# Kernel tuning notes

Measured on AMD Instinct MI355X. Metric: run time of the kernel, lower is better.

The kernel has to match this reference:

```python
import jax, jax.numpy as jnp
import numpy as np

DIM = 512
HEADS = 4
MARGIN = 1.0


def _attn_pool(x, Wq, bq, Wk, bk, Wv, bv, Wo, bo):
    # SelfAttention(video_dim, m_dim=DIM, heads=HEADS) followed by mean over time
    B, T, _ = x.shape
    hd = DIM // HEADS
    q = (x @ Wq + bq).reshape(B, T, HEADS, hd)
    k = (x @ Wk + bk).reshape(B, T, HEADS, hd)
    v = (x @ Wv + bv).reshape(B, T, HEADS, hd)
    a = jax.nn.softmax(jnp.einsum('bthd,bshd->bhts', q, k) / jnp.sqrt(jnp.float32(hd)), axis=-1)
    out = jnp.einsum('bhts,bshd->bthd', a, v).reshape(B, T, DIM) @ Wo + bo
    return out.mean(axis=1)  # [B, DIM]


def _ranking(x1, x2, gmask, margin):
    # vectorized form of the per-row torch.roll loop:
    # s[i, b] = <x1[b], x2[(b - i) mod B]>
    B = x1.shape[0]
    idx = (jnp.arange(B)[None, :] - jnp.arange(B)[:, None]) % B  # [B, B]
    s = jnp.einsum('bc,ibc->ib', x1, x2[idx])                    # [B, B]
    mask = gmask[idx] & gmask[None, :]                           # [B, B]
    # max-margin ranking loss with per-column masked mean, then mean over valid cols
    loss = jnp.maximum(0.0, margin + s[1:] - s[0:1])             # [B-1, B]
    m = mask[1:]
    cnt = m.sum(axis=0)
    col_mean = jnp.where(cnt > 0, (loss * m).sum(axis=0) / jnp.maximum(cnt, 1), 0.0)
    valid = cnt > 0
    loss_val = jnp.sum(col_mean * valid) / jnp.maximum(valid.sum(), 1)
    # ranking accuracy: idx==0 iff the true (row 0) score is max among selected
    sel_sum = jnp.sum(jnp.where(mask, s, 0.0), axis=0)
    col_valid = (sel_sum != 0) & mask.any(axis=0)
    s_masked = jnp.where(mask, s, -jnp.inf)
    top_is_first = (s[0] >= s_masked.max(axis=0)).astype(jnp.float32)
    acc = jnp.sum(jnp.where(col_valid, top_is_first, 0.0)) / jnp.maximum(col_valid.sum(), 1)
    return loss_val, jax.lax.stop_gradient(acc)


def setup_inputs() -> dict:
    key = jax.random.key(0)
    ks = iter(jax.random.split(key, 64))

    def nrm(shape, s=0.02):
        return jax.random.normal(next(ks), shape, jnp.float32) * s

    inp = {
        'o': jax.random.normal(next(ks), (128, 1024, DIM), jnp.float32),
        'rgb': jax.random.normal(next(ks), (128, 64, 2048), jnp.float32),
        'audio': jax.random.normal(next(ks), (128, 64, 128), jnp.float32),
        'group_mask': jax.random.randint(next(ks), (128,), 0, 2).astype(bool),
    }
    for name, d in (('rgb', 2048), ('audio', 128)):
        inp[f'{name}_Wq'] = nrm((d, DIM)); inp[f'{name}_bq'] = jnp.zeros((DIM,), jnp.float32)
        inp[f'{name}_Wk'] = nrm((d, DIM)); inp[f'{name}_bk'] = jnp.zeros((DIM,), jnp.float32)
        inp[f'{name}_Wv'] = nrm((d, DIM)); inp[f'{name}_bv'] = jnp.zeros((DIM,), jnp.float32)
        inp[f'{name}_Wo'] = nrm((DIM, DIM)); inp[f'{name}_bo'] = jnp.zeros((DIM,), jnp.float32)
        inp[f'{name}_W2'] = nrm((DIM, DIM)); inp[f'{name}_b2'] = jnp.zeros((DIM,), jnp.float32)
    inp['expand_W'] = nrm((DIM, 2 * DIM))
    inp['expand_b'] = jnp.zeros((2 * DIM,), jnp.float32)
    return inp


def reference(o, rgb, audio, group_mask,
              rgb_Wq, rgb_bq, rgb_Wk, rgb_bk, rgb_Wv, rgb_bv, rgb_Wo, rgb_bo, rgb_W2, rgb_b2,
              audio_Wq, audio_bq, audio_Wk, audio_bk, audio_Wv, audio_bv, audio_Wo, audio_bo,
              audio_W2, audio_b2, expand_W, expand_b):
    # per-modality encoders (CollaborativeGating multiplies are discarded in the
    # original forward, so gating is a no-op on the output -> skipped)
    f_rgb = _attn_pool(rgb, rgb_Wq, rgb_bq, rgb_Wk, rgb_bk, rgb_Wv, rgb_bv, rgb_Wo, rgb_bo) @ rgb_W2 + rgb_b2
    f_aud = _attn_pool(audio, audio_Wq, audio_bq, audio_Wk, audio_bk, audio_Wv, audio_bv, audio_Wo, audio_bo) @ audio_W2 + audio_b2
    feat = jnp.concatenate([f_rgb, f_aud], axis=-1)  # [B, 2*DIM]
    oo = o.mean(axis=-2) @ expand_W + expand_b       # [B, 2*DIM]
    oo = oo / jnp.maximum(jnp.linalg.norm(oo, axis=-1, keepdims=True), 1e-12)
    l1, a1 = _ranking(oo, feat, group_mask, MARGIN)
    l2, a2 = _ranking(feat, oo, group_mask, MARGIN)
    loss = l1 + l2
    acc = (a1 + a2) / 2.0
    return loss, acc
```

## Files before the change

kernel.cpp:

```cpp
#include <hip/hip_runtime.h>
#include <hip/hip_bf16.h>
#include <math.h>


using bf16x8 = __attribute__((ext_vector_type(8))) __bf16;
using f32x4  = __attribute__((ext_vector_type(4))) float;

enum : size_t {
  B_PART = 0,
  B_OM   = B_PART + (size_t)128*16*2*512*4,
  B_OO   = B_OM   + (size_t)128*512*4,
  B_G    = B_OO   + (size_t)128*1024*4,
  B_PP   = B_G    + (size_t)128*128*4,
  B_PO   = B_PP   + (size_t)2*128*512*4,
  B_FEAT = B_PO   + (size_t)2*128*512*4,
  B_QBF  = B_FEAT + (size_t)2*128*512*4,
  B_KBF  = B_QBF  + (size_t)2*8192*512*2,
  B_VBF  = B_KBF  + (size_t)2*8192*512*2,
  B_XR   = B_VBF  + (size_t)2*8192*512*2,
  B_XA   = B_XR   + (size_t)8192*2048*2,
  B_WT   = B_XA   + (size_t)8192*128*2,
  B_END  = B_WT   + (size_t)3*512*2048*2 + (size_t)3*512*128*2
};

__device__ __forceinline__ unsigned short f2bf(float f) {
  __hip_bfloat16 h = __float2bfloat16(f);
  return __builtin_bit_cast(unsigned short, h);
}
__device__ __forceinline__ unsigned pack2(float a, float b) {
  return (unsigned)f2bf(a) | ((unsigned)f2bf(b) << 16);
}

struct PrepArgs {
  const float* xr; unsigned short* xrb;
  const float* xa; unsigned short* xab;
  const float* w[6];
  unsigned short* wt[6];
};

__device__ __forceinline__ void castT64(const float* __restrict__ W,
                                        unsigned short* __restrict__ Wt,
                                        int K, int n0, int k0, int tid) {
  __shared__ float t[64][65];
  int c = tid & 63, r4 = tid >> 6;
#pragma unroll
  for (int i = 0; i < 16; ++i) {
    int r = r4 * 16 + i;
    t[c][r] = W[(size_t)(k0 + r) * 512 + n0 + c];
  }
  __syncthreads();
  int nr = tid >> 3, kk = (tid & 7) * 8;
#pragma unroll
  for (int p = 0; p < 2; ++p) {
    int n = nr + p * 32;
    float4 x0 = *(const float4*)&t[n][kk];
    float4 x1 = *(const float4*)&t[n][kk + 4];
    uint4 pk;
    pk.x = pack2(x0.x, x0.y); pk.y = pack2(x0.z, x0.w);
    pk.z = pack2(x1.x, x1.y); pk.w = pack2(x1.z, x1.w);
    *(uint4*)&Wt[(size_t)(n0 + n) * K + k0 + kk] = pk;
  }
}

__device__ __forceinline__ void cast8(const float* __restrict__ x,
                                      unsigned short* __restrict__ y,
                                      int i, int stride, int total) {
  for (; i < total; i += stride) {
    float4 v0 = *(const float4*)(x + (size_t)i * 8);
    float4 v1 = *(const float4*)(x + (size_t)i * 8 + 4);
    uint4 pk;
    pk.x = pack2(v0.x, v0.y); pk.y = pack2(v0.z, v0.w);
    pk.z = pack2(v1.x, v1.y); pk.w = pack2(v1.z, v1.w);
    *(uint4*)(y + (size_t)i * 8) = pk;
  }
}

__global__ __launch_bounds__(256) void prep_k(PrepArgs a) {
  int bid = blockIdx.x, tid = threadIdx.x;
  if (bid < 768) {
    int w = bid >> 8, t = bid & 255;
    castT64(a.w[w], a.wt[w], 2048, (t >> 5) * 64, (t & 31) * 64, tid);
  } else if (bid < 816) {
    int t = bid - 768; int w = t >> 4; t &= 15;
    castT64(a.w[3 + w], a.wt[3 + w], 128, (t >> 1) * 64, (t & 1) * 64, tid);
  } else if (bid < 1840) {
    cast8(a.xr, a.xrb, (bid - 816) * 256 + tid, 262144, 2097152);
  } else {
    cast8(a.xa, a.xab, (bid - 1840) * 256 + tid, 16384, 131072);
  }
}

struct QkvAll {
  const unsigned short* A[2];
  const unsigned short* Wt[6];
  const float* bias[6];
  unsigned short* out[6];
  const float* o; float* part;
};

__device__ __forceinline__ void stage16(const void* g, void* l) {
  __builtin_amdgcn_global_load_lds((const __attribute__((address_space(1))) void*)g,
                                   (__attribute__((address_space(3))) void*)l, 16, 0, 0);
}

__global__ __launch_bounds__(256) void qkv_mean_k(QkvAll args) {
  __shared__ __align__(16) char smem[16384];

  int id = blockIdx.x;
  int blk = id / 448, off = id % 448;

  if (off >= 192) {
    int mb = blk * 256 + (off - 192);
    int c = mb & 15, b = mb >> 4;
    const float* base = args.o + ((size_t)b * 1024 + (size_t)c * 64) * 512;
    int tid = threadIdx.x;
    int d4 = (tid & 127) << 2, half = tid >> 7;
    float4 s = {0.f, 0.f, 0.f, 0.f};
    for (int t = half; t < 64; t += 2) {
      float4 v = *(const float4*)(base + (size_t)t * 512 + d4);
      s.x += v.x; s.y += v.y; s.z += v.z; s.w += v.w;
    }
    *(float4*)(args.part + (((size_t)b * 16 + c) * 2 + half) * 512 + d4) = s;
    return;
  }

  int qid = blk * 192 + off;
  unsigned short* As = (unsigned short*)smem;
  unsigned short* Bs = (unsigned short*)(smem + 8192);

  int mi = qid >= 768 ? 1 : 0; qid -= mi * 768;
  int by = qid & 63, bx = (qid >> 6) & 3, bz = qid >> 8;
  int K = mi ? 128 : 2048;
  const unsigned short* A = args.A[mi];
  int wi = mi * 3 + bz;
  const unsigned short* Bt = args.Wt[wi];
  const float* bias = args.bias[wi];

  int tid = threadIdx.x;
  int l = tid & 63, w = tid >> 6;
  int row0 = by * 128, col0 = bx * 128;
  int wrow = (w & 1) * 64, wcol = (w >> 1) * 64;
  int kg = l >> 4, lr = l & 15;

  f32x4 acc[4][4] = {};

  for (int k0 = 0; k0 < K; k0 += 32) {
#pragma unroll
    for (int i = 0; i < 2; ++i) {
      int c = w * 128 + i * 64 + l;
      int r = c >> 2, s = (c & 3) * 8;
      stage16(A + (size_t)(row0 + r) * K + k0 + s, smem + (size_t)(w * 128 + i * 64) * 16);
      stage16(Bt + (size_t)(col0 + r) * K + k0 + s, smem + 8192 + (size_t)(w * 128 + i * 64) * 16);
    }
    __syncthreads();
    bf16x8 af[4], bfr[4];
#pragma unroll
    for (int m = 0; m < 4; ++m) {
      af[m]  = *(const bf16x8*)(As + (size_t)(wrow + m * 16 + lr) * 32 + kg * 8);
      bfr[m] = *(const bf16x8*)(Bs + (size_t)(wcol + m * 16 + lr) * 32 + kg * 8);
    }
#pragma unroll
    for (int m = 0; m < 4; ++m)
#pragma unroll
      for (int n = 0; n < 4; ++n)
        acc[m][n] = __builtin_amdgcn_mfma_f32_16x16x32_bf16(af[m], bfr[n], acc[m][n], 0, 0, 0);
    __syncthreads();
  }

  float bv[4];
#pragma unroll
  for (int n = 0; n < 4; ++n) bv[n] = bias[col0 + wcol + n * 16 + lr];
  float* cst = (float*)(smem) + w * 1024;
  unsigned short* C = args.out[wi];
  int rr = l >> 3, q = l & 7;
#pragma unroll
  for (int m = 0; m < 4; ++m) {
#pragma unroll
    for (int n = 0; n < 4; ++n) {
      int g0 = (n * 16 + lr) >> 3, o0 = lr & 7;
#pragma unroll
      for (int j = 0; j < 4; ++j) {
        int row = kg * 4 + j;
        cst[row * 64 + (((g0 ^ (row & 7)) << 3) | o0)] = acc[m][n][j] + bv[n];
      }
    }
#pragma unroll
    for (int p = 0; p < 2; ++p) {
      int row = rr + p * 8;
      int grp = q ^ (row & 7);
      float4 x0 = *(const float4*)&cst[row * 64 + grp * 8];
      float4 x1 = *(const float4*)&cst[row * 64 + grp * 8 + 4];
      uint4 pk;
      pk.x = pack2(x0.x, x0.y); pk.y = pack2(x0.z, x0.w);
      pk.z = pack2(x1.x, x1.y); pk.w = pack2(x1.z, x1.w);
      *(uint4*)&C[(size_t)(row0 + wrow + m * 16 + row) * 512 + col0 + wcol + q * 8] = pk;
    }
  }
}

__global__ __launch_bounds__(512) void finalize_mean_k(const float* __restrict__ part,
                                                       float* __restrict__ om) {
  int b = blockIdx.x, d = threadIdx.x;
  float s = 0.f;
  for (int c = 0; c < 32; ++c) s += part[((size_t)b * 32 + c) * 512 + d];
  om[(size_t)b * 512 + d] = s * (1.f / 1024.f);
}

__global__ __launch_bounds__(256) void gemm_f32_k(
    const float* __restrict__ A, int lda,
    const float* __restrict__ W, int ldw,
    const float* __restrict__ bias,
    float* __restrict__ C, int ldc, int K) {
  __shared__ float As[16][65];
  __shared__ float Ws[16][64];
  int tid = threadIdx.x;
  int tx = tid & 15, ty = tid >> 4;
  int row0 = blockIdx.y * 64, col0 = blockIdx.x * 64;
  float acc[4][4] = {};
  int ar = tid >> 2, ac = (tid & 3) << 2;
  int wr = tid >> 4, wc = (tid & 15) << 2;
  for (int k0 = 0; k0 < K; k0 += 16) {
    float4 av = *(const float4*)(A + (size_t)(row0 + ar) * lda + k0 + ac);
    As[ac + 0][ar] = av.x; As[ac + 1][ar] = av.y;
    As[ac + 2][ar] = av.z; As[ac + 3][ar] = av.w;
    float4 wv = *(const float4*)(W + (size_t)(k0 + wr) * ldw + col0 + wc);
    *(float4*)&Ws[wr][wc] = wv;
    __syncthreads();
#pragma unroll
    for (int k = 0; k < 16; ++k) {
      float a0 = As[k][(ty << 2) + 0], a1 = As[k][(ty << 2) + 1];
      float a2 = As[k][(ty << 2) + 2], a3 = As[k][(ty << 2) + 3];
      float4 w = *(const float4*)&Ws[k][tx << 2];
      acc[0][0] += a0 * w.x; acc[0][1] += a0 * w.y; acc[0][2] += a0 * w.z; acc[0][3] += a0 * w.w;
      acc[1][0] += a1 * w.x; acc[1][1] += a1 * w.y; acc[1][2] += a1 * w.z; acc[1][3] += a1 * w.w;
      acc[2][0] += a2 * w.x; acc[2][1] += a2 * w.y; acc[2][2] += a2 * w.z; acc[2][3] += a2 * w.w;
      acc[3][0] += a3 * w.x; acc[3][1] += a3 * w.y; acc[3][2] += a3 * w.z; acc[3][3] += a3 * w.w;
    }
    __syncthreads();
  }
  float4 bv = *(const float4*)(bias + col0 + (tx << 2));
#pragma unroll
  for (int i = 0; i < 4; ++i) {
    float4 ov;
    ov.x = acc[i][0] + bv.x; ov.y = acc[i][1] + bv.y;
    ov.z = acc[i][2] + bv.z; ov.w = acc[i][3] + bv.w;
    *(float4*)(C + (size_t)(row0 + (ty << 2) + i) * ldc + col0 + (tx << 2)) = ov;
  }
}

__global__ __launch_bounds__(256) void gemm_f32_2w_k(
    const float* __restrict__ A,
    const float* __restrict__ W0, const float* __restrict__ W1,
    const float* __restrict__ b0, const float* __restrict__ b1,
    float* __restrict__ C) {
  const float* W = (blockIdx.y >= 2) ? W1 : W0;
  const float* bias = (blockIdx.y >= 2) ? b1 : b0;
  __shared__ float As[16][65];
  __shared__ float Ws[16][64];
  int tid = threadIdx.x;
  int tx = tid & 15, ty = tid >> 4;
  int row0 = blockIdx.y * 64, col0 = blockIdx.x * 64;
  float acc[4][4] = {};
  int ar = tid >> 2, ac = (tid & 3) << 2;
  int wr = tid >> 4, wc = (tid & 15) << 2;
  for (int k0 = 0; k0 < 512; k0 += 16) {
    float4 av = *(const float4*)(A + (size_t)(row0 + ar) * 512 + k0 + ac);
    As[ac + 0][ar] = av.x; As[ac + 1][ar] = av.y;
    As[ac + 2][ar] = av.z; As[ac + 3][ar] = av.w;
    float4 wv = *(const float4*)(W + (size_t)(k0 + wr) * 512 + col0 + wc);
    *(float4*)&Ws[wr][wc] = wv;
    __syncthreads();
#pragma unroll
    for (int k = 0; k < 16; ++k) {
      float a0 = As[k][(ty << 2) + 0], a1 = As[k][(ty << 2) + 1];
      float a2 = As[k][(ty << 2) + 2], a3 = As[k][(ty << 2) + 3];
      float4 w = *(const float4*)&Ws[k][tx << 2];
      acc[0][0] += a0 * w.x; acc[0][1] += a0 * w.y; acc[0][2] += a0 * w.z; acc[0][3] += a0 * w.w;
      acc[1][0] += a1 * w.x; acc[1][1] += a1 * w.y; acc[1][2] += a1 * w.z; acc[1][3] += a1 * w.w;
      acc[2][0] += a2 * w.x; acc[2][1] += a2 * w.y; acc[2][2] += a2 * w.z; acc[2][3] += a2 * w.w;
      acc[3][0] += a3 * w.x; acc[3][1] += a3 * w.y; acc[3][2] += a3 * w.z; acc[3][3] += a3 * w.w;
    }
    __syncthreads();
  }
  float4 bv = *(const float4*)(bias + col0 + (tx << 2));
#pragma unroll
  for (int i = 0; i < 4; ++i) {
    float4 ov;
    ov.x = acc[i][0] + bv.x; ov.y = acc[i][1] + bv.y;
    ov.z = acc[i][2] + bv.z; ov.w = acc[i][3] + bv.w;
    *(float4*)(C + (size_t)(row0 + (ty << 2) + i) * 512 + col0 + (tx << 2)) = ov;
  }
}

__global__ __launch_bounds__(256) void attn_pool_k(
    const unsigned short* __restrict__ qbf,
    const unsigned short* __restrict__ kbf,
    const unsigned short* __restrict__ vbf,
    float* __restrict__ pooled) {
  __shared__ float wlds[4][64];
  int b = blockIdx.x, m = blockIdx.y;
  int tid = threadIdx.x;
  int w = tid >> 6, l = tid & 63, lr = l & 15, g = l >> 4;
  size_t base = ((size_t)m * 8192 + (size_t)b * 64) * 512 + w * 128;

  bf16x8 qf[4][4];
#pragma unroll
  for (int tb = 0; tb < 4; ++tb)
#pragma unroll
    for (int ks = 0; ks < 4; ++ks)
      qf[tb][ks] = *(const bf16x8*)(qbf + base + (size_t)(tb * 16 + lr) * 512 + ks * 32 + g * 8);

  f32x4 acc[4][4] = {};
#pragma unroll
  for (int sb = 0; sb < 4; ++sb) {
    bf16x8 kf[4];
#pragma unroll
    for (int ks = 0; ks < 4; ++ks)
      kf[ks] = *(const bf16x8*)(kbf + base + (size_t)(sb * 16 + lr) * 512 + ks * 32 + g * 8);
#pragma unroll
    for (int tb = 0; tb < 4; ++tb)
#pragma unroll
      for (int ks = 0; ks < 4; ++ks)
        acc[sb][tb] = __builtin_amdgcn_mfma_f32_16x16x32_bf16(kf[ks], qf[tb][ks], acc[sb][tb], 0, 0, 0);
  }

  const float scale = 0.08838834764831845f;
  float mx[4] = {-INFINITY, -INFINITY, -INFINITY, -INFINITY};
#pragma unroll
  for (int sb = 0; sb < 4; ++sb)
#pragma unroll
    for (int tb = 0; tb < 4; ++tb)
#pragma unroll
      for (int j = 0; j < 4; ++j) {
        acc[sb][tb][j] *= scale;
        mx[tb] = fmaxf(mx[tb], acc[sb][tb][j]);
      }
#pragma unroll
  for (int tb = 0; tb < 4; ++tb) {
    mx[tb] = fmaxf(mx[tb], __shfl_xor(mx[tb], 16));
    mx[tb] = fmaxf(mx[tb], __shfl_xor(mx[tb], 32));
  }
  float sm[4] = {0.f, 0.f, 0.f, 0.f};
#pragma unroll
  for (int sb = 0; sb < 4; ++sb)
#pragma unroll
    for (int tb = 0; tb < 4; ++tb)
#pragma unroll
      for (int j = 0; j < 4; ++j) {
        float e = expf(acc[sb][tb][j] - mx[tb]);
        acc[sb][tb][j] = e;
        sm[tb] += e;
      }
  float inv[4];
#pragma unroll
  for (int tb = 0; tb < 4; ++tb) {
    sm[tb] += __shfl_xor(sm[tb], 16);
    sm[tb] += __shfl_xor(sm[tb], 32);
    inv[tb] = 1.f / sm[tb];
  }
#pragma unroll
  for (int sb = 0; sb < 4; ++sb)
#pragma unroll
    for (int j = 0; j < 4; ++j) {
      float cs = acc[sb][0][j] * inv[0] + acc[sb][1][j] * inv[1]
               + acc[sb][2][j] * inv[2] + acc[sb][3][j] * inv[3];
      cs += __shfl_xor(cs, 1);
      cs += __shfl_xor(cs, 2);
      cs += __shfl_xor(cs, 4);
      cs += __shfl_xor(cs, 8);
      if (lr == 0) wlds[w][sb * 16 + g * 4 + j] = cs * (1.f / 64.f);
    }
  __syncthreads();

  int h = tid >> 6, c2 = (tid & 63) << 1;
  size_t vbase = ((size_t)m * 8192 + (size_t)b * 64) * 512 + h * 128 + c2;
  float s0 = 0.f, s1 = 0.f;
#pragma unroll 8
  for (int s = 0; s < 64; ++s) {
    unsigned u = *(const unsigned*)(vbf + vbase + (size_t)s * 512);
    float vlo = __builtin_bit_cast(float, u << 16);
    float vhi = __builtin_bit_cast(float, u & 0xffff0000u);
    float wv = wlds[h][s];
    s0 += wv * vlo; s1 += wv * vhi;
  }
  float2 o2 = {s0, s1};
  *(float2*)(pooled + ((size_t)m * 128 + b) * 512 + h * 128 + c2) = o2;
}

__global__ __launch_bounds__(256) void ntg_k(const float* __restrict__ oo,
                                             const float* __restrict__ feat,
                                             float* __restrict__ G) {
  __shared__ float As[16][33], Bs[16][33];
  __shared__ float inv32[32];
  int tid = threadIdx.x;
  int row0 = blockIdx.y * 32, col0 = blockIdx.x * 32;
  int ar = tid >> 3, aq = tid & 7;
  int ty = tid >> 4, tx = tid & 15;
  float acc[2][2] = {};
  float ssq = 0.f;
  for (int k0 = 0; k0 < 1024; k0 += 16) {
    float2 av = *(const float2*)(oo + (size_t)(row0 + ar) * 1024 + k0 + aq * 2);
    As[aq * 2 + 0][ar] = av.x;
    As[aq * 2 + 1][ar] = av.y;
    ssq += av.x * av.x + av.y * av.y;
    int kk = k0 + aq * 2;
    float2 bv = *(const float2*)(feat + (size_t)((kk >> 9) * 128 + col0 + ar) * 512 + (kk & 511));
    Bs[aq * 2 + 0][ar] = bv.x;
    Bs[aq * 2 + 1][ar] = bv.y;
    __syncthreads();
#pragma unroll
    for (int k = 0; k < 16; ++k) {
      float a0 = As[k][ty * 2], a1 = As[k][ty * 2 + 1];
      float b0 = Bs[k][tx * 2], b1 = Bs[k][tx * 2 + 1];
      acc[0][0] += a0 * b0; acc[0][1] += a0 * b1;
      acc[1][0] += a1 * b0; acc[1][1] += a1 * b1;
    }
    __syncthreads();
  }
  ssq += __shfl_xor(ssq, 1);
  ssq += __shfl_xor(ssq, 2);
  ssq += __shfl_xor(ssq, 4);
  if (aq == 0) inv32[ar] = 1.f / fmaxf(sqrtf(ssq), 1e-12f);
  __syncthreads();
#pragma unroll
  for (int i = 0; i < 2; ++i)
#pragma unroll
    for (int j = 0; j < 2; ++j)
      G[(size_t)(row0 + ty * 2 + i) * 128 + col0 + tx * 2 + j] = acc[i][j] * inv32[ty * 2 + i];
}

__global__ __launch_bounds__(128) void final_k(const float* __restrict__ G,
                                               const int* __restrict__ gmask,
                                               float* __restrict__ out) {
  __shared__ float cm[2][128], vd[2][128], tp[2][128], cv[2][128];
  __shared__ int gm[128];
  int b = threadIdx.x;
  gm[b] = gmask[b];
  __syncthreads();
  for (int r = 0; r < 2; ++r) {
    bool gb = gm[b] != 0;
    float s0 = G[b * 128 + b];
    int cnt = 0;
    float lsum = 0.f, selsum = 0.f, smax = -INFINITY;
    bool anym = false;
    for (int i = 0; i < 128; ++i) {
      int j = (b - i + 128) & 127;
      bool mk = gb && (gm[j] != 0);
      float sv = (r == 0) ? G[b * 128 + j] : G[j * 128 + b];
      if (mk) {
        selsum += sv; anym = true;
        smax = fmaxf(smax, sv);
        if (i >= 1) { cnt++; lsum += fmaxf(0.f, 1.f + sv - s0); }
      }
    }
    cm[r][b] = (cnt > 0) ? (lsum / (float)cnt) : 0.f;
    vd[r][b] = (cnt > 0) ? 1.f : 0.f;
    bool colvalid = (selsum != 0.f) && anym;
    tp[r][b] = (colvalid && (s0 >= smax)) ? 1.f : 0.f;
    cv[r][b] = colvalid ? 1.f : 0.f;
  }
  __syncthreads();
  if (b == 0) {
    float loss = 0.f, acc = 0.f;
    for (int r = 0; r < 2; ++r) {
      float scm = 0, svd = 0, stp = 0, scv = 0;
      for (int i = 0; i < 128; ++i) { scm += cm[r][i]; svd += vd[r][i]; stp += tp[r][i]; scv += cv[r][i]; }
      loss += scm / fmaxf(svd, 1.f);
      acc += stp / fmaxf(scv, 1.f);
    }
    out[0] = loss;
    out[1] = acc * 0.5f;
  }
}

extern "C" void kernel_launch(void* const* d_in, const int* in_sizes, int n_in,
                              void* d_out, int out_size, void* d_ws, size_t ws_size,
                              hipStream_t stream) {
  const float* o     = (const float*)d_in[0];
  const float* rgb   = (const float*)d_in[1];
  const float* audio = (const float*)d_in[2];
  const int* gmask   = (const int*)d_in[3];
  const float* W[2][10];
  for (int m = 0; m < 2; ++m)
    for (int w = 0; w < 10; ++w) W[m][w] = (const float*)d_in[4 + m * 10 + w];
  const float* expand_W = (const float*)d_in[24];
  const float* expand_b = (const float*)d_in[25];

  char* ws = (char*)d_ws;
  float* part = (float*)(ws + B_PART);
  float* om   = (float*)(ws + B_OM);
  float* oo   = (float*)(ws + B_OO);
  float* G    = (float*)(ws + B_G);
  float* pp2  = (float*)(ws + B_PP);
  float* po2  = (float*)(ws + B_PO);
  float* feat2= (float*)(ws + B_FEAT);
  unsigned short* qbf = (unsigned short*)(ws + B_QBF);
  unsigned short* kbf = (unsigned short*)(ws + B_KBF);
  unsigned short* vbf = (unsigned short*)(ws + B_VBF);
  unsigned short* xrb = (unsigned short*)(ws + B_XR);
  unsigned short* xab = (unsigned short*)(ws + B_XA);
  unsigned short* wt  = (unsigned short*)(ws + B_WT);
  unsigned short* wtp[6];
  wtp[0] = wt;
  wtp[1] = wtp[0] + (size_t)512 * 2048;
  wtp[2] = wtp[1] + (size_t)512 * 2048;
  wtp[3] = wtp[2] + (size_t)512 * 2048;
  wtp[4] = wtp[3] + (size_t)512 * 128;
  wtp[5] = wtp[4] + (size_t)512 * 128;

  PrepArgs pa;
  pa.xr = rgb;   pa.xrb = xrb;
  pa.xa = audio; pa.xab = xab;
  pa.w[0] = W[0][0]; pa.w[1] = W[0][2]; pa.w[2] = W[0][4];
  pa.w[3] = W[1][0]; pa.w[4] = W[1][2]; pa.w[5] = W[1][4];
  for (int i = 0; i < 6; ++i) pa.wt[i] = wtp[i];
  prep_k<<<1904, 256, 0, stream>>>(pa);

  QkvAll qa;
  qa.A[0] = xrb; qa.A[1] = xab;
  for (int i = 0; i < 6; ++i) qa.Wt[i] = wtp[i];
  qa.bias[0] = W[0][1]; qa.bias[1] = W[0][3]; qa.bias[2] = W[0][5];
  qa.bias[3] = W[1][1]; qa.bias[4] = W[1][3]; qa.bias[5] = W[1][5];
  qa.out[0] = qbf;                       qa.out[1] = kbf;                       qa.out[2] = vbf;
  qa.out[3] = qbf + (size_t)8192 * 512;  qa.out[4] = kbf + (size_t)8192 * 512;  qa.out[5] = vbf + (size_t)8192 * 512;
  qa.o = o; qa.part = part;
  qkv_mean_k<<<3584, 256, 0, stream>>>(qa);

  finalize_mean_k<<<128, 512, 0, stream>>>(part, om);
  gemm_f32_k<<<dim3(16, 2), 256, 0, stream>>>(om, 512, expand_W, 1024, expand_b, oo, 1024, 512);

  attn_pool_k<<<dim3(128, 2), 256, 0, stream>>>(qbf, kbf, vbf, pp2);

  gemm_f32_2w_k<<<dim3(8, 4), 256, 0, stream>>>(pp2, W[0][6], W[1][6], W[0][7], W[1][7], po2);
  gemm_f32_2w_k<<<dim3(8, 4), 256, 0, stream>>>(po2, W[0][8], W[1][8], W[0][9], W[1][9], feat2);

  ntg_k<<<dim3(4, 4), 256, 0, stream>>>(oo, feat2, G);
  final_k<<<1, 128, 0, stream>>>(G, gmask, (float*)d_out);
}
```

Baseline: 393.6 us.

## Double-buffer QKV GEMM LDS staging with XOR-swizzled layout

The QKV projection GEMM now keeps two 16KB LDS buffers and issues the global-to-LDS loads for the next K tile before computing on the current one. It waits only for the older loads with a partial vmcnt instead of a full __syncthreads. The staged data is also XOR-swizzled so that the fragment reads from LDS avoid bank conflicts, and the bias load is hoisted ahead of the loop. The cost is twice the shared memory per block, which can lower occupancy, plus hand-written waitcnt and barrier code that has to stay correct.

```diff
diff --git a/kernel.cpp b/kernel.cpp
--- a/kernel.cpp
+++ b/kernel.cpp
@@ -104,7 +104,7 @@
 }
 
 __global__ __launch_bounds__(256) void qkv_mean_k(QkvAll args) {
-  __shared__ __align__(16) char smem[16384];
+  __shared__ __align__(16) char smem[32768];
 
   int id = blockIdx.x;
   int blk = id / 448, off = id % 448;
@@ -125,12 +125,10 @@
   }
 
   int qid = blk * 192 + off;
-  unsigned short* As = (unsigned short*)smem;
-  unsigned short* Bs = (unsigned short*)(smem + 8192);
-
   int mi = qid >= 768 ? 1 : 0; qid -= mi * 768;
   int by = qid & 63, bx = (qid >> 6) & 3, bz = qid >> 8;
   int K = mi ? 128 : 2048;
+  int nt = K >> 5;
   const unsigned short* A = args.A[mi];
   int wi = mi * 3 + bz;
   const unsigned short* Bt = args.Wt[wi];
@@ -142,34 +140,60 @@
   int wrow = (w & 1) * 64, wcol = (w >> 1) * 64;
   int kg = l >> 4, lr = l & 15;
 
-  f32x4 acc[4][4] = {};
-
-  for (int k0 = 0; k0 < K; k0 += 32) {
+  float bv[4];
+#pragma unroll
+  for (int n = 0; n < 4; ++n) bv[n] = bias[col0 + wcol + n * 16 + lr];
+  asm volatile("" :: "v"(bv[0]), "v"(bv[1]), "v"(bv[2]), "v"(bv[3]));
+
+  auto stage_pair = [&](char* dbuf, int k0s) {
 #pragma unroll
     for (int i = 0; i < 2; ++i) {
       int c = w * 128 + i * 64 + l;
-      int r = c >> 2, s = (c & 3) * 8;
-      stage16(A + (size_t)(row0 + r) * K + k0 + s, smem + (size_t)(w * 128 + i * 64) * 16);
-      stage16(Bt + (size_t)(col0 + r) * K + k0 + s, smem + 8192 + (size_t)(w * 128 + i * 64) * 16);
-    }
-    __syncthreads();
+      int B_ = c << 4;
+      int e6 = ((B_ >> 6) ^ (B_ >> 8)) & 1;
+      int E  = B_ ^ (e6 << 4) ^ (((B_ >> 7) & 1) << 5) ^ (((B_ >> 8) & 1) << 6);
+      int r = E >> 6, s = ((E >> 4) & 3) << 3;
+      stage16(A + (size_t)(row0 + r) * K + k0s + s, dbuf + (w * 128 + i * 64) * 16);
+      stage16(Bt + (size_t)(col0 + r) * K + k0s + s, dbuf + 8192 + (w * 128 + i * 64) * 16);
+    }
+  };
+
+  f32x4 acc[4][4] = {};
+  int xorA = (lr & 7) << 4;
+
+  stage_pair(smem, 0);
+  int cur = 0;
+  for (int t = 0; t < nt; ++t) {
+    if (t + 1 < nt) {
+      stage_pair(smem + ((cur ^ 1) << 14), (t + 1) << 5);
+      asm volatile("s_waitcnt vmcnt(4)" ::: "memory");
+    } else {
+      asm volatile("s_waitcnt vmcnt(0)" ::: "memory");
+    }
+    __builtin_amdgcn_s_barrier();
+    __builtin_amdgcn_sched_barrier(0);
+
+    const char* Ab = smem + (cur << 14);
+    const char* Bb = Ab + 8192;
     bf16x8 af[4], bfr[4];
 #pragma unroll
     for (int m = 0; m < 4; ++m) {
-      af[m]  = *(const bf16x8*)(As + (size_t)(wrow + m * 16 + lr) * 32 + kg * 8);
-      bfr[m] = *(const bf16x8*)(Bs + (size_t)(wcol + m * 16 + lr) * 32 + kg * 8);
+      int ra = wrow + m * 16 + lr;
+      int rb = wcol + m * 16 + lr;
+      af[m]  = *(const bf16x8*)(Ab + (((ra << 6) + (kg << 4)) ^ xorA));
+      bfr[m] = *(const bf16x8*)(Bb + (((rb << 6) + (kg << 4)) ^ xorA));
     }
 #pragma unroll
     for (int m = 0; m < 4; ++m)
 #pragma unroll
       for (int n = 0; n < 4; ++n)
         acc[m][n] = __builtin_amdgcn_mfma_f32_16x16x32_bf16(af[m], bfr[n], acc[m][n], 0, 0, 0);
-    __syncthreads();
-  }
-
-  float bv[4];
-#pragma unroll
-  for (int n = 0; n < 4; ++n) bv[n] = bias[col0 + wcol + n * 16 + lr];
+
+    __builtin_amdgcn_sched_barrier(0);
+    __builtin_amdgcn_s_barrier();
+    cur ^= 1;
+  }
+
   float* cst = (float*)(smem) + w * 1024;
   unsigned short* C = args.out[wi];
   int rr = l >> 3, q = l & 7;
```

New measurement: 382.6 us (median of 2 runs). -2.8%, faster.
